# Performance work log

Measured on AMD Instinct MI355X. Metric: run time of the kernel, lower is better.

Reference implementation:

```python
import jax, jax.numpy as jnp
import numpy as np

EMBED = 768
HEADS = 12
HEAD_DIM = EMBED // HEADS
HIDDEN = 4 * EMBED
EPS = 1e-5


def _layernorm(x, w, b):
    mu = jnp.mean(x, axis=-1, keepdims=True)
    var = jnp.mean(jnp.square(x - mu), axis=-1, keepdims=True)
    return (x - mu) * jax.lax.rsqrt(var + EPS) * w + b


def setup_inputs() -> dict:
    key = jax.random.key(0)
    ks = jax.random.split(key, 12)
    s = 0.02
    return {
        "x": jax.random.normal(ks[0], (2, 2048, EMBED), dtype=jnp.float32),
        "ln1_w": jnp.ones((EMBED,), jnp.float32),
        "ln1_b": jnp.zeros((EMBED,), jnp.float32),
        "qkv_w": jax.random.normal(ks[1], (3 * EMBED, EMBED), jnp.float32) * s,
        "qkv_b": jnp.zeros((3 * EMBED,), jnp.float32),
        "proj_w": jax.random.normal(ks[2], (EMBED, EMBED), jnp.float32) * s,
        "proj_b": jnp.zeros((EMBED,), jnp.float32),
        "ln2_w": jnp.ones((EMBED,), jnp.float32),
        "ln2_b": jnp.zeros((EMBED,), jnp.float32),
        "fc1_w": jax.random.normal(ks[3], (HIDDEN, EMBED), jnp.float32) * s,
        "fc1_b": jnp.zeros((HIDDEN,), jnp.float32),
        "fc2_w": jax.random.normal(ks[4], (EMBED, HIDDEN), jnp.float32) * s,
        "fc2_b": jnp.zeros((EMBED,), jnp.float32),
    }


def reference(x, ln1_w, ln1_b, qkv_w, qkv_b, proj_w, proj_b,
              ln2_w, ln2_b, fc1_w, fc1_b, fc2_w, fc2_b):
    B, N, C = x.shape
    scale = float(HEAD_DIM) ** 0.5  # NOTE: module MULTIPLIES by sqrt(head_dim)

    # --- attention branch ---
    h = _layernorm(x, ln1_w, ln1_b)
    qkv = h @ qkv_w.T + qkv_b                     # [B,N,3C]
    qkv = qkv.reshape(B, N, 3, HEADS, HEAD_DIM)
    q = qkv[:, :, 0].transpose(0, 2, 1, 3)        # [B,H,N,D]
    k = qkv[:, :, 1].transpose(0, 2, 1, 3)
    v = qkv[:, :, 2].transpose(0, 2, 1, 3)
    attn = jnp.einsum('bhnd,bhmd->bhnm', q, k) * scale
    attn = jax.nn.softmax(attn, axis=-1)
    o = jnp.einsum('bhnm,bhmd->bhnd', attn, v)    # [B,H,N,D]
    o = o.transpose(0, 2, 1, 3).reshape(B, N, C)
    x = x + (o @ proj_w.T + proj_b)

    # --- MLP branch ---
    h = _layernorm(x, ln2_w, ln2_b)
    h = jax.nn.gelu(h @ fc1_w.T + fc1_b, approximate=False)
    x = x + (h @ fc2_w.T + fc2_b)
    return x
```

## Files before the change

### kernel.cpp

```cpp
#include <hip/hip_runtime.h>
#include <hip/hip_bf16.h>

typedef __attribute__((ext_vector_type(8))) short short8;
typedef __attribute__((ext_vector_type(4))) float f32x4;
typedef __attribute__((ext_vector_type(4))) int i32x4;

__device__ inline unsigned short f2bs(float f) {
  union { float f; unsigned u; } v; v.f = f;
  unsigned r = v.u + 0x7fff + ((v.u >> 16) & 1);
  return (unsigned short)(r >> 16);
}

__device__ inline float bs2f(unsigned short u) {
  union { unsigned u; float f; } c; c.u = (unsigned)u << 16; return c.f;
}

__device__ inline unsigned pkbf(float a, float b) {
  __hip_bfloat162 h = __float22bfloat162_rn(float2{a, b});
  union { __hip_bfloat162 h; unsigned u; } c; c.h = h;
  return c.u;
}

__device__ inline float exp2v(float x) {
  float r; asm("v_exp_f32 %0, %1" : "=v"(r) : "v"(x)); return r;
}

__device__ inline float max3f(float a, float b, float c) {
  return fmaxf(fmaxf(a, b), c);
}

__device__ inline void gload16(const void* g, void* l) {
  __builtin_amdgcn_global_load_lds((const __attribute__((address_space(1))) void*)g,
                                   (__attribute__((address_space(3))) void*)l,
                                   16, 0, 0);
}

__global__ __launch_bounds__(256)
void cvt_all(const float* __restrict__ s0, const float* __restrict__ s1,
             const float* __restrict__ s2, const float* __restrict__ s3,
             unsigned short* __restrict__ d0, unsigned short* __restrict__ d1,
             unsigned short* __restrict__ d2, unsigned short* __restrict__ d3)
{
  size_t i = (size_t)blockIdx.x * 256 + threadIdx.x;
  const float* src; unsigned short* dst;
  if (i < 442368) { src = s0; dst = d0; }
  else if (i < 589824) { src = s1; dst = d1; i -= 442368; }
  else if (i < 1179648) { src = s2; dst = d2; i -= 589824; }
  else { src = s3; dst = d3; i -= 1179648; }
  float4 v = ((const float4*)src)[i];
  ushort4 o;
  o.x = f2bs(v.x); o.y = f2bs(v.y); o.z = f2bs(v.z); o.w = f2bs(v.w);
  ((ushort4*)dst)[i] = o;
}

__global__ __launch_bounds__(256)
void ln_kernel(const float* __restrict__ x, const float* __restrict__ w,
               const float* __restrict__ bsh, unsigned short* __restrict__ out)
{
  const int row = blockIdx.x;
  const float* xr = x + (size_t)row * 768;
  float v[3];
  float s = 0.f, sq = 0.f;
#pragma unroll
  for (int i = 0; i < 3; ++i) {
    v[i] = xr[threadIdx.x + i * 256];
    s += v[i]; sq += v[i] * v[i];
  }
#pragma unroll
  for (int d = 1; d < 64; d <<= 1) {
    s  += __shfl_xor(s, d, 64);
    sq += __shfl_xor(sq, d, 64);
  }
  __shared__ float ss[4], ssq[4];
  const int wv = threadIdx.x >> 6;
  if ((threadIdx.x & 63) == 0) { ss[wv] = s; ssq[wv] = sq; }
  __syncthreads();
  s  = ss[0] + ss[1] + ss[2] + ss[3];
  sq = ssq[0] + ssq[1] + ssq[2] + ssq[3];
  const float mu = s * (1.0f / 768.0f);
  const float var = sq * (1.0f / 768.0f) - mu * mu;
  const float rstd = rsqrtf(var + 1e-5f);
#pragma unroll
  for (int i = 0; i < 3; ++i) {
    const int c = threadIdx.x + i * 256;
    out[(size_t)row * 768 + c] = f2bs((v[i] - mu) * rstd * w[c] + bsh[c]);
  }
}

__global__ __launch_bounds__(256)
void reduce_ln2(const unsigned short* __restrict__ p, const float* __restrict__ bias,
                const float* __restrict__ resid, const float* __restrict__ lw,
                const float* __restrict__ lb, float* __restrict__ x2,
                unsigned short* __restrict__ h)
{
  const size_t MN = 4096ull * 768;
  const int row = blockIdx.x;
  const size_t r0 = (size_t)row * 768;
  float v[3];
  float s = 0.f, sq = 0.f;
#pragma unroll
  for (int i = 0; i < 3; ++i) {
    const int c = threadIdx.x + i * 256;
    const float a = bs2f(p[r0 + c]) + bs2f(p[MN + r0 + c]) + bias[c] + resid[r0 + c];
    x2[r0 + c] = a;
    v[i] = a; s += a; sq += a * a;
  }
#pragma unroll
  for (int d = 1; d < 64; d <<= 1) {
    s  += __shfl_xor(s, d, 64);
    sq += __shfl_xor(sq, d, 64);
  }
  __shared__ float ss[4], ssq[4];
  const int wv = threadIdx.x >> 6;
  if ((threadIdx.x & 63) == 0) { ss[wv] = s; ssq[wv] = sq; }
  __syncthreads();
  s  = ss[0] + ss[1] + ss[2] + ss[3];
  sq = ssq[0] + ssq[1] + ssq[2] + ssq[3];
  const float mu = s * (1.0f / 768.0f);
  const float var = sq * (1.0f / 768.0f) - mu * mu;
  const float rstd = rsqrtf(var + 1e-5f);
#pragma unroll
  for (int i = 0; i < 3; ++i) {
    const int c = threadIdx.x + i * 256;
    h[r0 + c] = f2bs((v[i] - mu) * rstd * lw[c] + lb[c]);
  }
}

template<int S>
__global__ __launch_bounds__(256)
void reduce_k(const unsigned short* __restrict__ p, const float* __restrict__ bias,
              const float* __restrict__ resid, float* __restrict__ out)
{
  const size_t MN = 4096ull * 768;
  const size_t i = ((size_t)blockIdx.x * 256 + threadIdx.x) * 4;
  float ax = 0.f, ay = 0.f, az = 0.f, aw = 0.f;
#pragma unroll
  for (int s = 0; s < S; ++s) {
    ushort4 b = *(const ushort4*)(p + s * MN + i);
    ax += bs2f(b.x); ay += bs2f(b.y); az += bs2f(b.z); aw += bs2f(b.w);
  }
  const int col = (int)(i % 768);
  float4 bb = *(const float4*)(bias + col);
  float4 rr = *(const float4*)(resid + i);
  float4 r;
  r.x = ax + bb.x + rr.x; r.y = ay + bb.y + rr.y;
  r.z = az + bb.z + rr.z; r.w = aw + bb.w + rr.w;
  *(float4*)(out + i) = r;
}

template<int EPI>
__global__ __launch_bounds__(256, 3)
void gemm_nt(const unsigned short* __restrict__ A,
             const unsigned short* __restrict__ Bw,
             const float* __restrict__ bias,
             const float* __restrict__ resid,
             void* __restrict__ out0, void* __restrict__ out1, void* __restrict__ out2,
             int M, int N, int Kslice, int Kstride)
{
  __shared__ __align__(1024) unsigned short As[3][4096];
  __shared__ __align__(1024) unsigned short Bs[3][4096];
  const int tid = threadIdx.x;
  const int lane = tid & 63;
  const int w = tid >> 6;
  const int wr = w >> 1, wc = w & 1;
  const int l15 = lane & 15, g = lane >> 4;

  const int nwg = gridDim.x * gridDim.y;
  const int hw = blockIdx.y * gridDim.x + blockIdx.x;
  const int virt = (hw & 7) * (nwg >> 3) + (hw >> 3);
  const int m0 = (virt / gridDim.x) * 128;
  const int n0 = (virt % gridDim.x) * 128;
  const int kbase = blockIdx.z * Kslice;

  f32x4 acc[4][4];
#pragma unroll
  for (int m = 0; m < 4; ++m)
#pragma unroll
    for (int n = 0; n < 4; ++n)
      acc[m][n] = (f32x4){0.f, 0.f, 0.f, 0.f};

  auto stage = [&](int buf, int k0) {
#pragma unroll
    for (int i = 0; i < 2; ++i) {
      const int f = w * 2 + i;
      gload16(A  + (size_t)(m0 + f * 16 + l15) * Kstride + kbase + k0 + g * 8,
              (char*)&As[buf][0] + f * 1024);
      gload16(Bw + (size_t)(n0 + f * 16 + l15) * Kstride + kbase + k0 + g * 8,
              (char*)&Bs[buf][0] + f * 1024);
    }
  };

  const int NT = Kslice >> 5;
  stage(0, 0);
  stage(1, 32);

  for (int t = 0; t < NT; ++t) {
    const int buf = t % 3;
    if (t + 1 < NT) {
      asm volatile("s_waitcnt vmcnt(4)" ::: "memory");
    } else {
      asm volatile("s_waitcnt vmcnt(0)" ::: "memory");
    }
    __builtin_amdgcn_s_barrier();
    asm volatile("" ::: "memory");
    if (t + 2 < NT) stage((t + 2) % 3, (t + 2) * 32);

    short8 af[4], bfr[4];
#pragma unroll
    for (int m = 0; m < 4; ++m)
      af[m] = *(const short8*)((const char*)&As[buf][0] + (wr * 4 + m) * 1024 + lane * 16);
#pragma unroll
    for (int n = 0; n < 4; ++n)
      bfr[n] = *(const short8*)((const char*)&Bs[buf][0] + (wc * 4 + n) * 1024 + lane * 16);
#pragma unroll
    for (int m = 0; m < 4; ++m)
#pragma unroll
      for (int n = 0; n < 4; ++n)
        acc[m][n] = __builtin_amdgcn_mfma_f32_16x16x32_bf16(af[m], bfr[n], acc[m][n], 0, 0, 0);
    asm volatile("" ::: "memory");
  }

#pragma unroll
  for (int m = 0; m < 4; ++m) {
    const int gmBase = m0 + wr * 64 + m * 16 + g * 4;
#pragma unroll
    for (int n = 0; n < 4; ++n) {
      const int gn = n0 + wc * 64 + n * 16 + l15;
      const float bval = (EPI == 4) ? 0.0f : bias[gn];
      float vj[4];
#pragma unroll
      for (int j = 0; j < 4; ++j) vj[j] = acc[m][n][j] + bval;
      if (EPI == 0) {
        const int three = gn / 768;
        const int hh = (gn % 768) >> 6;
        const int d = gn & 63;
        const int bb = gmBase >> 11, t = gmBase & 2047;
        if (three == 2) {
          ushort4 pk;
          pk.x = f2bs(vj[0]); pk.y = f2bs(vj[1]); pk.z = f2bs(vj[2]); pk.w = f2bs(vj[3]);
          const int kt = t & 63;
          const size_t pos = ((((size_t)(bb * 12 + hh) * 32 + (t >> 6)) * 8 + (d >> 4) * 2 + (kt >> 5)) * 64
                              + ((kt >> 2) & 3) * 16 + (d & 15)) * 8 + ((kt >> 4) & 1) * 4;
          *(ushort4*)((unsigned short*)out2 + pos) = pk;
        } else {
          unsigned short* dst = (three == 0) ? (unsigned short*)out0 : (unsigned short*)out1;
#pragma unroll
          for (int j = 0; j < 4; ++j) {
            float v = vj[j];
            if (three == 0) v *= 11.5415603f;
            dst[(((size_t)bb * 12 + hh) * 2048 + (t + j)) * 64 + d] = f2bs(v);
          }
        }
      } else if (EPI == 1 || EPI == 3) {
#pragma unroll
        for (int j = 0; j < 4; ++j) {
          const int gm = gmBase + j;
          ((float*)out0)[(size_t)gm * N + gn] = vj[j] + resid[(size_t)gm * N + gn];
        }
      } else if (EPI == 2) {
#pragma unroll
        for (int j = 0; j < 4; ++j) {
          const int gm = gmBase + j;
          const float vv = vj[j];
          const float u = vv * (1.0f + 0.044715f * vv * vv);
          const float E = exp2v(2.0f * 0.7978845608f * 1.4426950409f * u);
          const float ge = vv - vv / (1.0f + E);
          ((unsigned short*)out0)[(size_t)gm * N + gn] = f2bs(ge);
        }
      } else {
        unsigned short* po = (unsigned short*)out0 + (size_t)blockIdx.z * M * N;
#pragma unroll
        for (int j = 0; j < 4; ++j) {
          const int gm = gmBase + j;
          po[(size_t)gm * N + gn] = f2bs(vj[j]);
        }
      }
    }
  }
}

template<int SPLIT>
__global__ __launch_bounds__(256, 6)
void attn_fwd(const unsigned short* __restrict__ Q,
              const unsigned short* __restrict__ K,
              const unsigned short* __restrict__ Vf,
              unsigned short* __restrict__ O,
              unsigned short* __restrict__ Op, float* __restrict__ Mb, float* __restrict__ Lb)
{
  __shared__ __align__(1024) unsigned short Ks[4096];
  __shared__ __align__(1024) unsigned short Vs[2][4096];
  const int tid = threadIdx.x, lane = tid & 63, w = tid >> 6;
  const int l15 = lane & 15, g = lane >> 4;

  const int hw = blockIdx.y * gridDim.x + blockIdx.x;
  const int virt = (hw & 7) * 96 + (hw >> 3);
  const int qblk = virt & 31;
  const int bh = virt >> 5;
  const int b = bh / 12, h = bh % 12;
  const int q0 = qblk * 64;
  const int half = SPLIT ? blockIdx.z : 0;
  const int NT = SPLIT ? 16 : 32;
  const int T0 = half * 16;
  const unsigned short* Qb = Q  + (size_t)bh * 2048 * 64;
  const unsigned short* Kb = K  + (size_t)bh * 2048 * 64;
  const unsigned short* Vb = Vf + (size_t)bh * 2048 * 64;

  const int qr = q0 + w * 16 + l15;
  short8 qf[2];
  qf[0] = *(const short8*)(Qb + (size_t)qr * 64 + g * 8);
  qf[1] = *(const short8*)(Qb + (size_t)qr * 64 + 32 + g * 8);

  float m_run = -1e30f, l_part = 0.f;
  f32x4 o_acc[4];
#pragma unroll
  for (int dc = 0; dc < 4; ++dc) o_acc[dc] = (f32x4){0.f, 0.f, 0.f, 0.f};

  auto stageK = [&](int gt) {
    const int kb = gt * 64;
#pragma unroll
    for (int i = 0; i < 2; ++i) {
      const int f = w * 2 + i;
      const int n = f >> 1, kc = f & 1;
      gload16(Kb + (size_t)(kb + n * 16 + l15) * 64 + kc * 32 + g * 8,
              (char*)&Ks[0] + f * 1024);
    }
  };
  auto stageV = [&](int buf, int gt) {
#pragma unroll
    for (int i = 0; i < 2; ++i) {
      const int chunk = tid + i * 256;
      gload16(Vb + (size_t)gt * 4096 + chunk * 8,
              (char*)&Vs[buf][0] + chunk * 16);
    }
  };

  stageK(T0);
  stageV(0, T0);

  for (int t = 0; t < NT; ++t) {
    const int vbuf = t & 1;
    asm volatile("s_waitcnt vmcnt(0)" ::: "memory");
    __builtin_amdgcn_s_barrier();
    asm volatile("" ::: "memory");
    if (t + 1 < NT) stageV(vbuf ^ 1, T0 + t + 1);

    f32x4 s2[4];
#pragma unroll
    for (int n = 0; n < 4; ++n) s2[n] = (f32x4){0.f, 0.f, 0.f, 0.f};
    __builtin_amdgcn_s_setprio(1);
#pragma unroll
    for (int n = 0; n < 4; ++n) {
      short8 kf0 = *(const short8*)(&Ks[(n * 2 + 0) * 512 + lane * 8]);
      short8 kf1 = *(const short8*)(&Ks[(n * 2 + 1) * 512 + lane * 8]);
      s2[n] = __builtin_amdgcn_mfma_f32_16x16x32_bf16(kf0, qf[0], s2[n], 0, 0, 0);
      s2[n] = __builtin_amdgcn_mfma_f32_16x16x32_bf16(kf1, qf[1], s2[n], 0, 0, 0);
    }
    __builtin_amdgcn_s_setprio(0);

    asm volatile("" ::: "memory");
    __builtin_amdgcn_s_barrier();
    asm volatile("" ::: "memory");
    if (t + 1 < NT) stageK(T0 + t + 1);

    float mx = max3f(max3f(s2[0][0], s2[0][1], s2[0][2]),
                     max3f(s2[0][3], s2[1][0], s2[1][1]),
                     max3f(s2[1][2], s2[1][3], s2[2][0]));
    mx = max3f(mx, max3f(s2[2][1], s2[2][2], s2[2][3]),
                   max3f(s2[3][0], s2[3][1], fmaxf(s2[3][2], s2[3][3])));
    mx = fmaxf(mx, __shfl_xor(mx, 16, 64));
    mx = fmaxf(mx, __shfl_xor(mx, 32, 64));
    if (__any(mx > m_run + 8.0f)) {
      const float mn = fmaxf(m_run, mx);
      const float alpha = exp2v(m_run - mn);
      m_run = mn;
      l_part *= alpha;
#pragma unroll
      for (int j = 0; j < 4; ++j) {
        const float aB = __shfl(alpha, (lane & 48) | (g * 4 + j), 64);
#pragma unroll
        for (int dc = 0; dc < 4; ++dc) o_acc[dc][j] *= aB;
      }
    }
    float e[4][4];
    float rs = 0.f;
#pragma unroll
    for (int n = 0; n < 4; ++n)
#pragma unroll
      for (int j = 0; j < 4; ++j) {
        e[n][j] = exp2v(s2[n][j] - m_run);
        rs += e[n][j];
      }
    l_part += rs;

    unsigned pw[2][4];
#pragma unroll
    for (int kc = 0; kc < 2; ++kc) {
      pw[kc][0] = pkbf(e[2 * kc][0],     e[2 * kc][1]);
      pw[kc][1] = pkbf(e[2 * kc][2],     e[2 * kc][3]);
      pw[kc][2] = pkbf(e[2 * kc + 1][0], e[2 * kc + 1][1]);
      pw[kc][3] = pkbf(e[2 * kc + 1][2], e[2 * kc + 1][3]);
    }

    const char* vsb = (const char*)&Vs[vbuf][0];
    __builtin_amdgcn_s_setprio(1);
#pragma unroll
    for (int kc = 0; kc < 2; ++kc) {
      i32x4 pt; pt.x = (int)pw[kc][0]; pt.y = (int)pw[kc][1]; pt.z = (int)pw[kc][2]; pt.w = (int)pw[kc][3];
      short8 pf = *(short8*)&pt;
#pragma unroll
      for (int dc = 0; dc < 4; ++dc) {
        short8 vfr = *(const short8*)(vsb + (((dc * 2 + kc) * 64 + lane) * 16));
        o_acc[dc] = __builtin_amdgcn_mfma_f32_16x16x32_bf16(pf, vfr, o_acc[dc], 0, 0, 0);
      }
    }
    __builtin_amdgcn_s_setprio(0);
    asm volatile("" ::: "memory");
  }

  l_part += __shfl_xor(l_part, 16, 64);
  l_part += __shfl_xor(l_part, 32, 64);
  if (SPLIT) {
    const int rowBase = (half * 24 + bh) * 2048;
    if (g == 0) {
      const int qm = q0 + w * 16 + l15;
      Mb[rowBase + qm] = m_run;
      Lb[rowBase + qm] = l_part;
    }
#pragma unroll
    for (int j = 0; j < 4; ++j) {
      const int row = q0 + w * 16 + g * 4 + j;
#pragma unroll
      for (int dc = 0; dc < 4; ++dc)
        Op[(size_t)(rowBase + row) * 64 + dc * 16 + l15] = f2bs(o_acc[dc][j]);
    }
  } else {
#pragma unroll
    for (int j = 0; j < 4; ++j) {
      const float lB = __shfl(l_part, (lane & 48) | (g * 4 + j), 64);
      const float inv = 1.0f / lB;
      const int qrow = q0 + w * 16 + g * 4 + j;
#pragma unroll
      for (int dc = 0; dc < 4; ++dc)
        O[((size_t)b * 2048 + qrow) * 768 + h * 64 + dc * 16 + l15] = f2bs(o_acc[dc][j] * inv);
    }
  }
}

__global__ __launch_bounds__(256)
void attn_combine(const unsigned short* __restrict__ Op, const float* __restrict__ Mb,
                  const float* __restrict__ Lb, unsigned short* __restrict__ O)
{
  const int idx = blockIdx.x * 256 + threadIdx.x;
  const int e4 = idx * 4;
  const int row = e4 >> 6;
  const int d0 = e4 & 63;
  const float m1 = Mb[row], m2 = Mb[49152 + row];
  const float l1 = Lb[row], l2 = Lb[49152 + row];
  const float mm = fmaxf(m1, m2);
  const float w1 = exp2v(m1 - mm), w2 = exp2v(m2 - mm);
  const float inv = 1.0f / (l1 * w1 + l2 * w2);
  ushort4 a1 = *(const ushort4*)(Op + (size_t)row * 64 + d0);
  ushort4 a2 = *(const ushort4*)(Op + 49152ull * 64 + (size_t)row * 64 + d0);
  ushort4 r;
  r.x = f2bs((bs2f(a1.x) * w1 + bs2f(a2.x) * w2) * inv);
  r.y = f2bs((bs2f(a1.y) * w1 + bs2f(a2.y) * w2) * inv);
  r.z = f2bs((bs2f(a1.z) * w1 + bs2f(a2.z) * w2) * inv);
  r.w = f2bs((bs2f(a1.w) * w1 + bs2f(a2.w) * w2) * inv);
  const int bh = row >> 11, q = row & 2047;
  const int b = bh / 12, hh = bh % 12;
  *(ushort4*)(O + ((size_t)(b * 2048 + q)) * 768 + hh * 64 + d0) = r;
}

extern "C" void kernel_launch(void* const* d_in, const int* in_sizes, int n_in,
                              void* d_out, int out_size, void* d_ws, size_t ws_size,
                              hipStream_t stream)
{
  const float* x      = (const float*)d_in[0];
  const float* ln1_w  = (const float*)d_in[1];
  const float* ln1_b  = (const float*)d_in[2];
  const float* qkv_w  = (const float*)d_in[3];
  const float* qkv_b  = (const float*)d_in[4];
  const float* proj_w = (const float*)d_in[5];
  const float* proj_b = (const float*)d_in[6];
  const float* ln2_w  = (const float*)d_in[7];
  const float* ln2_b  = (const float*)d_in[8];
  const float* fc1_w  = (const float*)d_in[9];
  const float* fc1_b  = (const float*)d_in[10];
  const float* fc2_w  = (const float*)d_in[11];
  const float* fc2_b  = (const float*)d_in[12];

  char* base = (char*)d_ws;
  size_t off = 0;
  auto take = [&](size_t bytes) {
    void* r = base + off;
    off = (off + bytes + 255) & ~(size_t)255;
    return r;
  };
  unsigned short* wq = (unsigned short*)take(2304ull * 768 * 2);
  unsigned short* wp = (unsigned short*)take(768ull * 768 * 2);
  unsigned short* w1 = (unsigned short*)take(3072ull * 768 * 2);
  unsigned short* w2 = (unsigned short*)take(768ull * 3072 * 2);
  unsigned short* h  = (unsigned short*)take(4096ull * 768 * 2);
  float* x2          = (float*)take(4096ull * 768 * 4);
  char* big          = (char*)take(4096ull * 3072 * 2);
  unsigned short* Qb = (unsigned short*)big;
  unsigned short* Kb = (unsigned short*)(big + 4096ull * 768 * 2);
  unsigned short* Vb = (unsigned short*)(big + 2ull * 4096 * 768 * 2);
  unsigned short* a2 = (unsigned short*)big;
  unsigned short* part = (unsigned short*)take(4ull * 4096 * 768 * 2);
  float* Mb_         = (float*)take(2ull * 49152 * 4);
  float* Lb_         = (float*)take(2ull * 49152 * 4);
  const bool can_split = off <= ws_size;

  cvt_all<<<6912, 256, 0, stream>>>(qkv_w, proj_w, fc1_w, fc2_w, wq, wp, w1, w2);

  ln_kernel<<<4096, 256, 0, stream>>>(x, ln1_w, ln1_b, h);
  gemm_nt<0><<<dim3(18, 32), 256, 0, stream>>>(h, wq, qkv_b, nullptr, Qb, Kb, Vb, 4096, 2304, 768, 768);

  if (can_split) {
    attn_fwd<1><<<dim3(32, 24, 2), 256, 0, stream>>>(Qb, Kb, Vb, nullptr, part, Mb_, Lb_);
    attn_combine<<<3072, 256, 0, stream>>>(part, Mb_, Lb_, h);
  } else {
    attn_fwd<0><<<dim3(32, 24), 256, 0, stream>>>(Qb, Kb, Vb, h, nullptr, nullptr, nullptr);
  }

  if (can_split) {
    gemm_nt<4><<<dim3(6, 32, 2), 256, 0, stream>>>(h, wp, nullptr, nullptr, part, nullptr, nullptr, 4096, 768, 384, 768);
    reduce_ln2<<<4096, 256, 0, stream>>>(part, proj_b, x, ln2_w, ln2_b, x2, h);
  } else {
    gemm_nt<1><<<dim3(6, 32), 256, 0, stream>>>(h, wp, proj_b, x, x2, nullptr, nullptr, 4096, 768, 768, 768);
    ln_kernel<<<4096, 256, 0, stream>>>(x2, ln2_w, ln2_b, h);
  }

  gemm_nt<2><<<dim3(24, 32), 256, 0, stream>>>(h, w1, fc1_b, nullptr, a2, nullptr, nullptr, 4096, 3072, 768, 768);

  if (can_split) {
    gemm_nt<4><<<dim3(6, 32, 4), 256, 0, stream>>>(a2, w2, nullptr, nullptr, part, nullptr, nullptr, 4096, 768, 768, 3072);
    reduce_k<4><<<3072, 256, 0, stream>>>(part, fc2_b, x2, (float*)d_out);
  } else {
    gemm_nt<3><<<dim3(6, 32), 256, 0, stream>>>(a2, w2, fc2_b, x2, d_out, nullptr, nullptr, 4096, 768, 3072, 3072);
  }
}
```

Before: 220.6 us.

## Swizzle GEMM LDS tiles and pre-fragment K layout for contiguous attention loads

The GEMM staging now loads each row's four 16-byte chunks contiguously from global memory, with an XOR swizzle on the LDS chunk index, instead of strided per-lane fragment loads. The QKV epilogue writes K directly in the MFMA fragment order that the attention kernel expects, so attention can stage K with fully contiguous 16-byte loads, as it already does for V. The aim is better global coalescing and fewer LDS bank conflicts. In exchange, the K epilogue becomes scattered 2-byte stores, and the design depends on the pre-swizzled layouts matching exactly between producer and consumer.

```diff
diff --git a/kernel.cpp b/kernel.cpp
--- a/kernel.cpp
+++ b/kernel.cpp
@@ -157,8 +157,8 @@
              void* __restrict__ out0, void* __restrict__ out1, void* __restrict__ out2,
              int M, int N, int Kslice, int Kstride)
 {
-  __shared__ __align__(1024) unsigned short As[3][4096];
-  __shared__ __align__(1024) unsigned short Bs[3][4096];
+  __shared__ __align__(16) unsigned short As[3][128 * 32];
+  __shared__ __align__(16) unsigned short Bs[3][128 * 32];
   const int tid = threadIdx.x;
   const int lane = tid & 63;
   const int w = tid >> 6;
@@ -182,11 +182,11 @@
   auto stage = [&](int buf, int k0) {
 #pragma unroll
     for (int i = 0; i < 2; ++i) {
-      const int f = w * 2 + i;
-      gload16(A  + (size_t)(m0 + f * 16 + l15) * Kstride + kbase + k0 + g * 8,
-              (char*)&As[buf][0] + f * 1024);
-      gload16(Bw + (size_t)(n0 + f * 16 + l15) * Kstride + kbase + k0 + g * 8,
-              (char*)&Bs[buf][0] + f * 1024);
+      const int f = tid + i * 256;
+      const int row = f >> 2, c8 = f & 3;
+      const int sc = c8 ^ (row & 3);
+      gload16(A  + (size_t)(m0 + row) * Kstride + kbase + k0 + sc * 8, (char*)&As[buf][0] + f * 16);
+      gload16(Bw + (size_t)(n0 + row) * Kstride + kbase + k0 + sc * 8, (char*)&Bs[buf][0] + f * 16);
     }
   };
 
@@ -207,11 +207,15 @@
 
     short8 af[4], bfr[4];
 #pragma unroll
-    for (int m = 0; m < 4; ++m)
-      af[m] = *(const short8*)((const char*)&As[buf][0] + (wr * 4 + m) * 1024 + lane * 16);
-#pragma unroll
-    for (int n = 0; n < 4; ++n)
-      bfr[n] = *(const short8*)((const char*)&Bs[buf][0] + (wc * 4 + n) * 1024 + lane * 16);
+    for (int m = 0; m < 4; ++m) {
+      const int r = wr * 64 + m * 16 + l15;
+      af[m] = *(const short8*)((const char*)&As[buf][0] + ((size_t)r * 32 + (g ^ (r & 3)) * 8) * 2);
+    }
+#pragma unroll
+    for (int n = 0; n < 4; ++n) {
+      const int r = wc * 64 + n * 16 + l15;
+      bfr[n] = *(const short8*)((const char*)&Bs[buf][0] + ((size_t)r * 32 + (g ^ (r & 3)) * 8) * 2);
+    }
 #pragma unroll
     for (int m = 0; m < 4; ++m)
 #pragma unroll
@@ -242,13 +246,25 @@
           const size_t pos = ((((size_t)(bb * 12 + hh) * 32 + (t >> 6)) * 8 + (d >> 4) * 2 + (kt >> 5)) * 64
                               + ((kt >> 2) & 3) * 16 + (d & 15)) * 8 + ((kt >> 4) & 1) * 4;
           *(ushort4*)((unsigned short*)out2 + pos) = pk;
+        } else if (three == 1) {
+          unsigned short* dst = (unsigned short*)out1;
+          const int gt = t >> 6;
+          const int kt0 = t & 63;
+          const int fb = d >> 5;
+          const int ge = (d >> 3) & 3;
+          const int e = d & 7;
+          const size_t base9 = ((size_t)(bb * 12 + hh) * 32 + gt) * 8;
+#pragma unroll
+          for (int j = 0; j < 4; ++j) {
+            const int kt = kt0 + j;
+            const size_t pos = (base9 + (kt >> 4) * 2 + fb) * 512 + (ge * 16 + (kt & 15)) * 8 + e;
+            dst[pos] = f2bs(vj[j]);
+          }
         } else {
-          unsigned short* dst = (three == 0) ? (unsigned short*)out0 : (unsigned short*)out1;
+          unsigned short* dst = (unsigned short*)out0;
 #pragma unroll
           for (int j = 0; j < 4; ++j) {
-            float v = vj[j];
-            if (three == 0) v *= 11.5415603f;
-            dst[(((size_t)bb * 12 + hh) * 2048 + (t + j)) * 64 + d] = f2bs(v);
+            dst[(((size_t)bb * 12 + hh) * 2048 + (t + j)) * 64 + d] = f2bs(vj[j] * 11.5415603f);
           }
         }
       } else if (EPI == 1 || EPI == 3) {
@@ -282,7 +298,7 @@
 template<int SPLIT>
 __global__ __launch_bounds__(256, 6)
 void attn_fwd(const unsigned short* __restrict__ Q,
-              const unsigned short* __restrict__ K,
+              const unsigned short* __restrict__ Kf,
               const unsigned short* __restrict__ Vf,
               unsigned short* __restrict__ O,
               unsigned short* __restrict__ Op, float* __restrict__ Mb, float* __restrict__ Lb)
@@ -302,7 +318,7 @@
   const int NT = SPLIT ? 16 : 32;
   const int T0 = half * 16;
   const unsigned short* Qb = Q  + (size_t)bh * 2048 * 64;
-  const unsigned short* Kb = K  + (size_t)bh * 2048 * 64;
+  const unsigned short* Kb = Kf + (size_t)bh * 2048 * 64;
   const unsigned short* Vb = Vf + (size_t)bh * 2048 * 64;
 
   const int qr = q0 + w * 16 + l15;
@@ -316,21 +332,17 @@
   for (int dc = 0; dc < 4; ++dc) o_acc[dc] = (f32x4){0.f, 0.f, 0.f, 0.f};
 
   auto stageK = [&](int gt) {
-    const int kb = gt * 64;
 #pragma unroll
     for (int i = 0; i < 2; ++i) {
-      const int f = w * 2 + i;
-      const int n = f >> 1, kc = f & 1;
-      gload16(Kb + (size_t)(kb + n * 16 + l15) * 64 + kc * 32 + g * 8,
-              (char*)&Ks[0] + f * 1024);
+      const int chunk = tid + i * 256;
+      gload16(Kb + (size_t)gt * 4096 + chunk * 8, (char*)&Ks[0] + chunk * 16);
     }
   };
   auto stageV = [&](int buf, int gt) {
 #pragma unroll
     for (int i = 0; i < 2; ++i) {
       const int chunk = tid + i * 256;
-      gload16(Vb + (size_t)gt * 4096 + chunk * 8,
-              (char*)&Vs[buf][0] + chunk * 16);
+      gload16(Vb + (size_t)gt * 4096 + chunk * 8, (char*)&Vs[buf][0] + chunk * 16);
     }
   };
 
```

Measured after the change: 188.1 us. 1.17x faster.
